# Optimization experiments

Hardware: AMD Instinct MI355X
Metric: run time of the kernel (lower is better)

The kernel has to match this reference:

```python
import jax, jax.numpy as jnp
import numpy as np

B, S, D, H, DK, DFF, L = 4, 1024, 1024, 16, 64, 4096, 128

def setup_inputs() -> dict:
    key = jax.random.key(0)
    ks = jax.random.split(key, 20)
    stdv = 1.0 / np.sqrt(D)
    u = lambda k, shape, s=stdv: jax.random.uniform(k, shape, jnp.float32, -s, s)
    x = jax.random.normal(ks[0], (B, S, D), jnp.float32)
    causal = jnp.triu(jnp.ones((S, S), bool), 1)          # True = masked
    attn_mask = jnp.broadcast_to(causal, (B, S, S))
    return {
        "x": x,
        "attn_mask": attn_mask,
        "W_q": u(ks[1], (H * DK, D)), "b_q": jnp.zeros((H * DK,)),
        "W_k": u(ks[2], (H * DK, D)), "b_k": jnp.zeros((H * DK,)),
        "W_v": u(ks[3], (H * DK, D)), "b_v": jnp.zeros((H * DK,)),
        "W_o": u(ks[4], (D, H * DK)), "b_o": jnp.zeros((D,)),
        "W_rel": u(ks[5], (2 * L + 1, DK), 1.0 / np.sqrt(DK)),
        "ln1_alpha": jnp.ones((D,)), "ln1_bias": jnp.zeros((D,)),
        "ln2_alpha": jnp.ones((D,)), "ln2_bias": jnp.zeros((D,)),
        "W1": u(ks[6], (DFF, D)), "b1": jnp.zeros((DFF,)),
        "W2": u(ks[7], (D, DFF)), "b2": jnp.zeros((D,)),
    }

def _layer_norm(x, alpha, bias, eps=1e-5):
    # Faithful to source: (x - mean) / (std + eps), std is biased (unbiased=False)
    m = jnp.mean(x, axis=-1, keepdims=True)
    std = jnp.sqrt(jnp.mean((x - m) ** 2, axis=-1, keepdims=True))
    return alpha * (x - m) / (std + eps) + bias

def reference(x, attn_mask, W_q, b_q, W_k, b_k, W_v, b_v, W_o, b_o, W_rel,
              ln1_alpha, ln1_bias, ln2_alpha, ln2_bias, W1, b1, W2, b2):
    b, s, d = x.shape
    q = (x @ W_q.T + b_q).reshape(b, s, H, DK)
    k = (x @ W_k.T + b_k).reshape(b, s, H, DK)
    v = (x @ W_v.T + b_v).reshape(b, s, H, DK)
    # relative position bias table lookup -> [s, s, DK]
    idx = jnp.clip(jnp.arange(s)[:, None] - jnp.arange(s)[None, :], -L, L) + L
    pos = W_rel[idx]
    # NOTE: original uses rel_pos_k_emb for BOTH pos_key and pos_value (as in source).
    scores = jnp.einsum('bqnd,bknd->bnqk', q, k) + jnp.einsum('bqnd,qkd->bnqk', q, pos)
    scores = scores / np.sqrt(DK)
    scores = jnp.where(attn_mask[:, None, :, :], jnp.float32(-10000.0), scores)
    attn = jax.nn.softmax(scores, axis=-1)
    out = jnp.einsum('bnqk,bknd->bnqd', attn, v) + jnp.einsum('bnqk,qkd->bnqd', attn, pos)
    out = out.transpose(0, 2, 1, 3).reshape(b, s, H * DK)
    out = out @ W_o.T + b_o
    # post-LN transformer layer: LN(x + attn), then LN(h + FFN(h))
    h = _layer_norm(x + out, ln1_alpha, ln1_bias)
    f = jax.nn.relu(h @ W1.T + b1) @ W2.T + b2
    return _layer_norm(h + f, ln2_alpha, ln2_bias)
```

## Files before the change

### kernel.cpp

```cpp
#include <hip/hip_runtime.h>
#include <cmath>
#include <cstdint>

typedef __bf16 bf16;
typedef __bf16 bf16x8 __attribute__((ext_vector_type(8)));
typedef __bf16 bf16x4 __attribute__((ext_vector_type(4)));
typedef float f32x4 __attribute__((ext_vector_type(4)));

__device__ __forceinline__ void async_ld16(const void* g, void* l) {
  __builtin_amdgcn_global_load_lds(
      (__attribute__((address_space(1))) void*)(uintptr_t)g,
      (__attribute__((address_space(3))) void*)l, 16, 0, 0);
}

__global__ void cast_kernel(const float* __restrict__ in, bf16* __restrict__ out, int n4) {
  int i = blockIdx.x * blockDim.x + threadIdx.x;
  if (i >= n4) return;
  float4 v = ((const float4*)in)[i];
  bf16x4 o; o[0]=(bf16)v.x; o[1]=(bf16)v.y; o[2]=(bf16)v.z; o[3]=(bf16)v.w;
  ((bf16x4*)out)[i] = o;
}

template<int BM>
__device__ __forceinline__ void gemm_core(
    const bf16* __restrict__ A, const bf16* __restrict__ Bm, const float* __restrict__ bias,
    float* __restrict__ outF, bf16* __restrict__ outB,
    const float* __restrict__ residF, const bf16* __restrict__ residB,
    int N, int K, int relu, bf16* As, bf16* Bs)
{
  constexpr int MI = BM / 32;
  const int tid  = threadIdx.x;
  const int wave = tid >> 6, lane = tid & 63;
  const int lr = lane & 15, lq = lane >> 4;
  const int bm = blockIdx.x * BM, bn = blockIdx.y * 128;
  const int wm = (wave >> 1) * (BM / 2), wn = (wave & 1) * 64;
  const int srow = lane >> 2, scol = (lane & 3) * 8;

  const f32x4 fz = {0.f, 0.f, 0.f, 0.f};
  f32x4 acc[MI][4];
#pragma unroll
  for (int i = 0; i < MI; i++)
#pragma unroll
    for (int j = 0; j < 4; j++) acc[i][j] = fz;

  for (int k0 = 0; k0 < K; k0 += 32) {
    __syncthreads();
    if (BM == 128) {
#pragma unroll
      for (int cc = 0; cc < 2; ++cc) {
        int c = wave * 2 + cc;
        async_ld16(A + (size_t)(bm + c * 16 + srow) * K + k0 + scol, As + c * 512);
      }
    } else {
      async_ld16(A + (size_t)(bm + wave * 16 + srow) * K + k0 + scol, As + wave * 512);
    }
#pragma unroll
    for (int cc = 0; cc < 2; ++cc) {
      int c = wave * 2 + cc;
      async_ld16(Bm + (size_t)(bn + c * 16 + srow) * K + k0 + scol, Bs + c * 512);
    }
    __syncthreads();
    bf16x8 af[MI], bfr[4];
#pragma unroll
    for (int mi = 0; mi < MI; mi++) af[mi]  = *(const bf16x8*)(As + (wm + mi*16 + lr)*32 + lq*8);
#pragma unroll
    for (int ni = 0; ni < 4; ni++) bfr[ni] = *(const bf16x8*)(Bs + (wn + ni*16 + lr)*32 + lq*8);
#pragma unroll
    for (int mi = 0; mi < MI; mi++)
#pragma unroll
      for (int ni = 0; ni < 4; ni++)
        acc[mi][ni] = __builtin_amdgcn_mfma_f32_16x16x32_bf16(af[mi], bfr[ni], acc[mi][ni], 0, 0, 0);
  }

#pragma unroll
  for (int ni = 0; ni < 4; ni++) {
    int n = bn + wn + ni*16 + lr;
    float bv = bias ? bias[n] : 0.0f;
#pragma unroll
    for (int mi = 0; mi < MI; mi++) {
#pragma unroll
      for (int r = 0; r < 4; r++) {
        int m = bm + wm + mi*16 + lq*4 + r;
        size_t idx = (size_t)m * N + n;
        float v = acc[mi][ni][r] + bv;
        if (relu) v = fmaxf(v, 0.0f);
        if (residF) v += residF[idx];
        if (residB) v += (float)residB[idx];
        if (outF) outF[idx] = v;
        else      outB[idx] = (bf16)v;
      }
    }
  }
}

template<int BM>
__global__ __launch_bounds__(256) void gemm_bt(
    const bf16* A, const bf16* Bm, const float* bias,
    float* outF, bf16* outB, const float* residF, const bf16* residB,
    int N, int K, int relu)
{
  __shared__ bf16 As[BM * 32];
  __shared__ bf16 Bs[128 * 32];
  gemm_core<BM>(A, Bm, bias, outF, outB, residF, residB, N, K, relu, As, Bs);
}

__global__ __launch_bounds__(256) void gemm_qkv(
    const bf16* A, const bf16* Bq, const bf16* Bk, const bf16* Bv,
    const float* bq, const float* bk, const float* bv,
    bf16* Oq, bf16* Ok, bf16* Ov, int N, int K)
{
  __shared__ bf16 As[128 * 32];
  __shared__ bf16 Bs[128 * 32];
  const bf16* Bm  = blockIdx.z == 0 ? Bq : (blockIdx.z == 1 ? Bk : Bv);
  const float* bi = blockIdx.z == 0 ? bq : (blockIdx.z == 1 ? bk : bv);
  bf16* O         = blockIdx.z == 0 ? Oq : (blockIdx.z == 1 ? Ok : Ov);
  gemm_core<128>(A, Bm, bi, nullptr, O, nullptr, nullptr, N, K, 0, As, Bs);
}

#define S_LEN 1024
#define ROWSTR 1024

__global__ __launch_bounds__(256) void attn_kernel(
    const bf16* __restrict__ Qg, const bf16* __restrict__ Kg, const bf16* __restrict__ Vg,
    const float* __restrict__ Wrel, bf16* __restrict__ Og)
{
  __shared__ __align__(16) bf16 hist[64][136];
  __shared__ __align__(16) bf16 rel_s[64][132];
  __shared__ __align__(16) bf16 ovl[13824];
  bf16* K_s = ovl;
  bf16* V_T = ovl + 4608;
  bf16* p_s = ovl + 9216;
  bf16* Wr_n = ovl;
  bf16* Wr_t = ovl;

  const int tid = threadIdx.x;
  const int wave = tid >> 6, lane = tid & 63;
  const int lr = lane & 15, lq = lane >> 4;
  const int qblk = 15 - blockIdx.x;
  const int b = blockIdx.y >> 4, h = blockIdx.y & 15;
  const int q0 = qblk * 64;
  const int T = qblk + 1;
  const int nearStart = (T > 3) ? T - 3 : 0;
  const size_t rowbase = (size_t)b * S_LEN * ROWSTR + h * 64;

  for (int e = tid; e < 144 * 64; e += 256) {
    int t = e >> 6, d = e & 63;
    float v = (t <= 128) ? Wrel[(size_t)(128 + t) * 64 + d] : 0.0f;
    Wr_n[t * 72 + d] = (bf16)v;
  }
  for (int e = tid; e < 64 * 68; e += 256) ((uint*)hist)[e] = 0u;

  const int qfrow = q0 + wave * 16 + lr;
  bf16x8 qf[2];
#pragma unroll
  for (int c = 0; c < 2; c++)
    qf[c] = *(const bf16x8*)(Qg + rowbase + (size_t)qfrow * ROWSTR + c * 32 + lq * 8);

  __syncthreads();

  const f32x4 fz = {0.f, 0.f, 0.f, 0.f};
#pragma unroll
  for (int tt = 0; tt < 9; ++tt) {
    f32x4 a = fz;
#pragma unroll
    for (int c = 0; c < 2; c++) {
      bf16x8 wf = *(const bf16x8*)(Wr_n + (tt * 16 + lr) * 72 + c * 32 + lq * 8);
      a = __builtin_amdgcn_mfma_f32_16x16x32_bf16(qf[c], wf, a, 0, 0, 0);
    }
    int t = tt * 16 + lr;
    if (t < 132) {
#pragma unroll
      for (int r = 0; r < 4; r++) rel_s[wave * 16 + lq * 4 + r][t] = (bf16)a[r];
    }
  }
  asm volatile("s_waitcnt lgkmcnt(0)" ::: "memory");
  float relc[4];
#pragma unroll
  for (int r = 0; r < 4; r++) relc[r] = 0.125f * (float)rel_s[wave * 16 + lq * 4 + r][128];

  float l_i[4], h128[4];
  f32x4 acc_o[4];
#pragma unroll
  for (int r = 0; r < 4; r++) { l_i[r] = 0.0f; h128[r] = 0.0f; }
#pragma unroll
  for (int dt = 0; dt < 4; dt++) acc_o[dt] = fz;
  const int qrow0 = q0 + wave * 16 + lq * 4;

  const int kr0 = tid >> 3, kc0 = (tid & 7) * 8;
  const int vr0 = 2 * (tid & 31), vd0 = (tid >> 5) * 8;
  uint4 ka, kb, va, vb;
  {
    const bf16* kp = Kg + rowbase + (size_t)kr0 * ROWSTR + kc0;
    ka = *(const uint4*)kp; kb = *(const uint4*)(kp + 32 * ROWSTR);
    const bf16* vp = Vg + rowbase + (size_t)vr0 * ROWSTR + vd0;
    va = *(const uint4*)vp; vb = *(const uint4*)(vp + ROWSTR);
  }

  for (int kt = 0; kt < T; ++kt) {
    const int k0 = kt * 64;
    __syncthreads();
    *(uint4*)(K_s + kr0 * 72 + kc0) = ka;
    *(uint4*)(K_s + (kr0 + 32) * 72 + kc0) = kb;
    {
      const ushort* pa = (const ushort*)&va;
      const ushort* pb = (const ushort*)&vb;
#pragma unroll
      for (int j = 0; j < 8; j++) {
        uint w = (uint)pa[j] | ((uint)pb[j] << 16);
        *(uint*)(V_T + (vd0 + j) * 72 + vr0) = w;
      }
    }
    __syncthreads();
    if (kt + 1 < T) {
      const bf16* kp = Kg + rowbase + (size_t)(k0 + 64 + kr0) * ROWSTR + kc0;
      ka = *(const uint4*)kp; kb = *(const uint4*)(kp + 32 * ROWSTR);
      const bf16* vp = Vg + rowbase + (size_t)(k0 + 64 + vr0) * ROWSTR + vd0;
      va = *(const uint4*)vp; vb = *(const uint4*)(vp + ROWSTR);
    }

    f32x4 sc[4];
#pragma unroll
    for (int nt = 0; nt < 4; nt++) {
      sc[nt] = fz;
#pragma unroll
      for (int c = 0; c < 2; c++) {
        bf16x8 kf = *(const bf16x8*)(K_s + (nt * 16 + lr) * 72 + c * 32 + lq * 8);
        sc[nt] = __builtin_amdgcn_mfma_f32_16x16x32_bf16(qf[c], kf, sc[nt], 0, 0, 0);
      }
    }

    float pw[4][4];
    if (kt < nearStart) {
#pragma unroll
      for (int nt = 0; nt < 4; nt++)
#pragma unroll
        for (int r = 0; r < 4; r++)
          pw[nt][r] = __expf(fmaf(sc[nt][r], 0.125f, relc[r]));
#pragma unroll
      for (int r = 0; r < 4; r++) {
        float s4 = pw[0][r] + pw[1][r] + pw[2][r] + pw[3][r];
        l_i[r] += s4; h128[r] += s4;
      }
    } else {
#pragma unroll
      for (int nt = 0; nt < 4; nt++) {
        int kg = k0 + nt * 16 + lr;
#pragma unroll
        for (int r = 0; r < 4; r++) {
          int qg = qrow0 + r;
          float p = 0.0f;
          if (kg <= qg) {
            int t = qg - kg; int tc = t > 128 ? 128 : t;
            p = __expf((sc[nt][r] + (float)rel_s[wave * 16 + lq * 4 + r][tc]) * 0.125f);
            l_i[r] += p;
            if (t >= 128) h128[r] += p;
            else          hist[wave * 16 + lq * 4 + r][t] = (bf16)p;
          }
          pw[nt][r] = p;
        }
      }
    }

#pragma unroll
    for (int nt = 0; nt < 4; nt++)
#pragma unroll
      for (int r = 0; r < 4; r++)
        p_s[(wave * 16 + lq * 4 + r) * 72 + nt * 16 + lr] = (bf16)pw[nt][r];
    asm volatile("s_waitcnt lgkmcnt(0)" ::: "memory");
#pragma unroll
    for (int c = 0; c < 2; c++) {
      bf16x8 pf = *(const bf16x8*)(p_s + (wave * 16 + lr) * 72 + c * 32 + lq * 8);
#pragma unroll
      for (int dt = 0; dt < 4; dt++) {
        bf16x8 vf = *(const bf16x8*)(V_T + (dt * 16 + lr) * 72 + c * 32 + lq * 8);
        acc_o[dt] = __builtin_amdgcn_mfma_f32_16x16x32_bf16(pf, vf, acc_o[dt], 0, 0, 0);
      }
    }
  }

  __syncthreads();
  for (int e = tid; e < 64 * 128; e += 256) {
    int d = e >> 7, t = e & 127;
    Wr_t[d * 136 + t] = (bf16)Wrel[(size_t)(128 + t) * 64 + d];
  }
  __syncthreads();
#pragma unroll
  for (int c = 0; c < 4; c++) {
    bf16x8 hf = *(const bf16x8*)&hist[wave * 16 + lr][c * 32 + lq * 8];
#pragma unroll
    for (int dt = 0; dt < 4; dt++) {
      bf16x8 wf = *(const bf16x8*)(Wr_t + (dt * 16 + lr) * 136 + c * 32 + lq * 8);
      acc_o[dt] = __builtin_amdgcn_mfma_f32_16x16x32_bf16(hf, wf, acc_o[dt], 0, 0, 0);
    }
  }
#pragma unroll
  for (int mk = 1; mk <= 8; mk <<= 1)
#pragma unroll
    for (int r = 0; r < 4; r++) {
      h128[r] += __shfl_xor(h128[r], mk);
      l_i[r]  += __shfl_xor(l_i[r],  mk);
    }
#pragma unroll
  for (int dt = 0; dt < 4; dt++) {
    float wv = Wrel[(size_t)256 * 64 + dt * 16 + lr];
#pragma unroll
    for (int r = 0; r < 4; r++) acc_o[dt][r] += h128[r] * wv;
  }
#pragma unroll
  for (int dt = 0; dt < 4; dt++)
#pragma unroll
    for (int r = 0; r < 4; r++) {
      int qg = qrow0 + r;
      float v = acc_o[dt][r] / l_i[r];
      Og[rowbase + (size_t)qg * ROWSTR + dt * 16 + lr] = (bf16)v;
    }
}

__global__ __launch_bounds__(256) void ln_kernel(
    const float* __restrict__ in, const float* __restrict__ alpha, const float* __restrict__ beta,
    float* __restrict__ outF, bf16* __restrict__ outB)
{
  const int row = blockIdx.x, tid = threadIdx.x;
  const int lane = tid & 63, wave = tid >> 6;
  float4 v = ((const float4*)(in + (size_t)row * 1024))[tid];
  float s  = v.x + v.y + v.z + v.w;
  float ss = v.x*v.x + v.y*v.y + v.z*v.z + v.w*v.w;
#pragma unroll
  for (int off = 32; off; off >>= 1) { s += __shfl_down(s, off); ss += __shfl_down(ss, off); }
  __shared__ float rs[4], rss[4];
  if (lane == 0) { rs[wave] = s; rss[wave] = ss; }
  __syncthreads();
  s  = rs[0] + rs[1] + rs[2] + rs[3];
  ss = rss[0] + rss[1] + rss[2] + rss[3];
  float mean = s * (1.0f / 1024.0f);
  float var  = ss * (1.0f / 1024.0f) - mean * mean;
  float inv  = 1.0f / (sqrtf(fmaxf(var, 0.0f)) + 1e-5f);
  float4 a = ((const float4*)alpha)[tid];
  float4 bb = ((const float4*)beta)[tid];
  float o0 = a.x * (v.x - mean) * inv + bb.x;
  float o1 = a.y * (v.y - mean) * inv + bb.y;
  float o2 = a.z * (v.z - mean) * inv + bb.z;
  float o3 = a.w * (v.w - mean) * inv + bb.w;
  if (outF) { float4 o = {o0, o1, o2, o3}; ((float4*)(outF + (size_t)row * 1024))[tid] = o; }
  if (outB) { bf16x4 o; o[0]=(bf16)o0; o[1]=(bf16)o1; o[2]=(bf16)o2; o[3]=(bf16)o3;
              ((bf16x4*)(outB + (size_t)row * 1024))[tid] = o; }
}

extern "C" void kernel_launch(void* const* d_in, const int* in_sizes, int n_in,
                              void* d_out, int out_size, void* d_ws, size_t ws_size,
                              hipStream_t stream) {
  (void)in_sizes; (void)n_in; (void)out_size; (void)ws_size;
  const int Mtok = 4096, D = 1024, DFF = 4096;

  const float* x    = (const float*)d_in[0];
  const float* Wq   = (const float*)d_in[2];
  const float* bq   = (const float*)d_in[3];
  const float* Wk   = (const float*)d_in[4];
  const float* bk   = (const float*)d_in[5];
  const float* Wv   = (const float*)d_in[6];
  const float* bv   = (const float*)d_in[7];
  const float* Wo   = (const float*)d_in[8];
  const float* bo   = (const float*)d_in[9];
  const float* Wrel = (const float*)d_in[10];
  const float* g1   = (const float*)d_in[11];
  const float* be1  = (const float*)d_in[12];
  const float* g2   = (const float*)d_in[13];
  const float* be2  = (const float*)d_in[14];
  const float* W1   = (const float*)d_in[15];
  const float* b1   = (const float*)d_in[16];
  const float* W2   = (const float*)d_in[17];
  const float* b2   = (const float*)d_in[18];

  char* ws = (char*)d_ws;
  const size_t MB = 1024 * 1024;
  bf16*  xb   = (bf16*)(ws + 0);
  bf16*  Wqb  = (bf16*)(ws + 8  * MB);
  bf16*  Wkb  = (bf16*)(ws + 10 * MB);
  bf16*  Wvb  = (bf16*)(ws + 12 * MB);
  bf16*  Wob  = (bf16*)(ws + 14 * MB);
  bf16*  W1b  = (bf16*)(ws + 16 * MB);
  bf16*  W2b  = (bf16*)(ws + 24 * MB);
  bf16*  Qb   = (bf16*)(ws + 32 * MB);
  bf16*  Kb   = (bf16*)(ws + 40 * MB);
  bf16*  Vb   = (bf16*)(ws + 48 * MB);
  bf16*  AOb  = (bf16*)(ws + 56 * MB);
  float* res1 = (float*)(ws + 64 * MB);
  bf16*  f1   = Qb;
  bf16*  hb   = xb;
  float* res2 = res1;

  cast_kernel<<<(Mtok * D / 4) / 256, 256, 0, stream>>>(x,  xb,  Mtok * D / 4);
  cast_kernel<<<(D * D / 4) / 256,    256, 0, stream>>>(Wq, Wqb, D * D / 4);
  cast_kernel<<<(D * D / 4) / 256,    256, 0, stream>>>(Wk, Wkb, D * D / 4);
  cast_kernel<<<(D * D / 4) / 256,    256, 0, stream>>>(Wv, Wvb, D * D / 4);
  cast_kernel<<<(D * D / 4) / 256,    256, 0, stream>>>(Wo, Wob, D * D / 4);
  cast_kernel<<<(DFF * D / 4) / 256,  256, 0, stream>>>(W1, W1b, DFF * D / 4);
  cast_kernel<<<(D * DFF / 4) / 256,  256, 0, stream>>>(W2, W2b, D * DFF / 4);

  gemm_qkv<<<dim3(32, 8, 3), 256, 0, stream>>>(xb, Wqb, Wkb, Wvb, bq, bk, bv, Qb, Kb, Vb, D, D);
  attn_kernel<<<dim3(16, 64), 256, 0, stream>>>(Qb, Kb, Vb, Wrel, AOb);
  gemm_bt<64><<<dim3(64, 8), 256, 0, stream>>>(AOb, Wob, bo, res1, nullptr, x, nullptr, D, D, 0);
  ln_kernel<<<Mtok, 256, 0, stream>>>(res1, g1, be1, nullptr, hb);
  gemm_bt<128><<<dim3(32, 32), 256, 0, stream>>>(hb, W1b, b1, nullptr, f1, nullptr, nullptr, DFF, D, 1);
  gemm_bt<64><<<dim3(64, 8), 256, 0, stream>>>(f1, W2b, b2, res2, nullptr, nullptr, hb, D, DFF, 0);
  ln_kernel<<<Mtok, 256, 0, stream>>>(res2, g2, be2, (float*)d_out, nullptr);
}
```

Before: 452.2 us.

## Split-K the N=1024 GEMMs into 128-row tiles and fuse reduction into LayerNorm

The output-projection and FFN-down GEMMs (N=1024) now run as a two-way split-K with 128-row tiles, writing two fp32 partial buffers. The LayerNorm kernel sums the partials and adds bias and residual before normalising, which replaces the old GEMM epilogue. All seven fp32-to-bf16 casts are merged into one launch. The intent is better MFMA tile efficiency and fewer launches, at the cost of an extra fp32 partial write and read per GEMM.

Result: faster. 417.5 us (-7.7%).

```diff
diff --git a/kernel.cpp b/kernel.cpp
--- a/kernel.cpp
+++ b/kernel.cpp
@@ -13,12 +13,25 @@
       (__attribute__((address_space(3))) void*)l, 16, 0, 0);
 }
 
-__global__ void cast_kernel(const float* __restrict__ in, bf16* __restrict__ out, int n4) {
-  int i = blockIdx.x * blockDim.x + threadIdx.x;
-  if (i >= n4) return;
-  float4 v = ((const float4*)in)[i];
+__global__ __launch_bounds__(256) void cast_all(
+    const float* __restrict__ x,  const float* __restrict__ wq, const float* __restrict__ wk,
+    const float* __restrict__ wv, const float* __restrict__ wo, const float* __restrict__ w1,
+    const float* __restrict__ w2,
+    bf16* xb, bf16* wqb, bf16* wkb, bf16* wvb, bf16* wob, bf16* w1b, bf16* w2b)
+{
+  int i = blockIdx.x * 256 + threadIdx.x;
+  const int M1 = 1 << 20, Q = 1 << 18;
+  const float* src; bf16* dst; int off;
+  if      (i < M1)            { src = x;  dst = xb;  off = i; }
+  else if (i < M1 + Q)        { src = wq; dst = wqb; off = i - M1; }
+  else if (i < M1 + 2 * Q)    { src = wk; dst = wkb; off = i - M1 - Q; }
+  else if (i < M1 + 3 * Q)    { src = wv; dst = wvb; off = i - M1 - 2 * Q; }
+  else if (i < M1 + 4 * Q)    { src = wo; dst = wob; off = i - M1 - 3 * Q; }
+  else if (i < 3 * M1)        { src = w1; dst = w1b; off = i - M1 - 4 * Q; }
+  else                        { src = w2; dst = w2b; off = i - 3 * M1; }
+  float4 v = ((const float4*)src)[off];
   bf16x4 o; o[0]=(bf16)v.x; o[1]=(bf16)v.y; o[2]=(bf16)v.z; o[3]=(bf16)v.w;
-  ((bf16x4*)out)[i] = o;
+  ((bf16x4*)dst)[off] = o;
 }
 
 template<int BM>
@@ -26,7 +39,7 @@
     const bf16* __restrict__ A, const bf16* __restrict__ Bm, const float* __restrict__ bias,
     float* __restrict__ outF, bf16* __restrict__ outB,
     const float* __restrict__ residF, const bf16* __restrict__ residB,
-    int N, int K, int relu, bf16* As, bf16* Bs)
+    int N, int kld, int kbeg, int kend, int relu, bf16* As, bf16* Bs)
 {
   constexpr int MI = BM / 32;
   const int tid  = threadIdx.x;
@@ -43,21 +56,21 @@
 #pragma unroll
     for (int j = 0; j < 4; j++) acc[i][j] = fz;
 
-  for (int k0 = 0; k0 < K; k0 += 32) {
+  for (int k0 = kbeg; k0 < kend; k0 += 32) {
     __syncthreads();
     if (BM == 128) {
 #pragma unroll
       for (int cc = 0; cc < 2; ++cc) {
         int c = wave * 2 + cc;
-        async_ld16(A + (size_t)(bm + c * 16 + srow) * K + k0 + scol, As + c * 512);
+        async_ld16(A + (size_t)(bm + c * 16 + srow) * kld + k0 + scol, As + c * 512);
       }
     } else {
-      async_ld16(A + (size_t)(bm + wave * 16 + srow) * K + k0 + scol, As + wave * 512);
+      async_ld16(A + (size_t)(bm + wave * 16 + srow) * kld + k0 + scol, As + wave * 512);
     }
 #pragma unroll
     for (int cc = 0; cc < 2; ++cc) {
       int c = wave * 2 + cc;
-      async_ld16(Bm + (size_t)(bn + c * 16 + srow) * K + k0 + scol, Bs + c * 512);
+      async_ld16(Bm + (size_t)(bn + c * 16 + srow) * kld + k0 + scol, Bs + c * 512);
     }
     __syncthreads();
     bf16x8 af[MI], bfr[4];
@@ -101,7 +114,17 @@
 {
   __shared__ bf16 As[BM * 32];
   __shared__ bf16 Bs[128 * 32];
-  gemm_core<BM>(A, Bm, bias, outF, outB, residF, residB, N, K, relu, As, Bs);
+  gemm_core<BM>(A, Bm, bias, outF, outB, residF, residB, N, K, 0, K, relu, As, Bs);
+}
+
+__global__ __launch_bounds__(256) void gemm_splitk(
+    const bf16* A, const bf16* Bm, float* part, int N, int kld, int kchunk)
+{
+  __shared__ bf16 As[128 * 32];
+  __shared__ bf16 Bs[128 * 32];
+  const int z = blockIdx.z;
+  gemm_core<128>(A, Bm, nullptr, part + (size_t)z * 4096 * N, nullptr, nullptr, nullptr,
+                 N, kld, z * kchunk, (z + 1) * kchunk, 0, As, Bs);
 }
 
 __global__ __launch_bounds__(256) void gemm_qkv(
@@ -114,7 +137,7 @@
   const bf16* Bm  = blockIdx.z == 0 ? Bq : (blockIdx.z == 1 ? Bk : Bv);
   const float* bi = blockIdx.z == 0 ? bq : (blockIdx.z == 1 ? bk : bv);
   bf16* O         = blockIdx.z == 0 ? Oq : (blockIdx.z == 1 ? Ok : Ov);
-  gemm_core<128>(A, Bm, bi, nullptr, O, nullptr, nullptr, N, K, 0, As, Bs);
+  gemm_core<128>(A, Bm, bi, nullptr, O, nullptr, nullptr, N, K, 0, K, 0, As, Bs);
 }
 
 #define S_LEN 1024
@@ -316,13 +339,29 @@
     }
 }
 
-__global__ __launch_bounds__(256) void ln_kernel(
-    const float* __restrict__ in, const float* __restrict__ alpha, const float* __restrict__ beta,
+__global__ __launch_bounds__(256) void ln_fuse(
+    const float* __restrict__ pA, const float* __restrict__ pB,
+    const float* __restrict__ bias,
+    const float* __restrict__ residF, const bf16* __restrict__ residB,
+    const float* __restrict__ alpha, const float* __restrict__ beta,
     float* __restrict__ outF, bf16* __restrict__ outB)
 {
   const int row = blockIdx.x, tid = threadIdx.x;
   const int lane = tid & 63, wave = tid >> 6;
-  float4 v = ((const float4*)(in + (size_t)row * 1024))[tid];
+  const size_t base = (size_t)row * 1024;
+  float4 v = ((const float4*)(pA + base))[tid];
+  float4 v2 = ((const float4*)(pB + base))[tid];
+  v.x += v2.x; v.y += v2.y; v.z += v2.z; v.w += v2.w;
+  float4 bv = ((const float4*)bias)[tid];
+  v.x += bv.x; v.y += bv.y; v.z += bv.z; v.w += bv.w;
+  if (residF) {
+    float4 rv = ((const float4*)(residF + base))[tid];
+    v.x += rv.x; v.y += rv.y; v.z += rv.z; v.w += rv.w;
+  }
+  if (residB) {
+    bf16x4 rv = ((const bf16x4*)(residB + base))[tid];
+    v.x += (float)rv[0]; v.y += (float)rv[1]; v.z += (float)rv[2]; v.w += (float)rv[3];
+  }
   float s  = v.x + v.y + v.z + v.w;
   float ss = v.x*v.x + v.y*v.y + v.z*v.z + v.w*v.w;
 #pragma unroll
@@ -341,16 +380,16 @@
   float o1 = a.y * (v.y - mean) * inv + bb.y;
   float o2 = a.z * (v.z - mean) * inv + bb.z;
   float o3 = a.w * (v.w - mean) * inv + bb.w;
-  if (outF) { float4 o = {o0, o1, o2, o3}; ((float4*)(outF + (size_t)row * 1024))[tid] = o; }
+  if (outF) { float4 o = {o0, o1, o2, o3}; ((float4*)(outF + base))[tid] = o; }
   if (outB) { bf16x4 o; o[0]=(bf16)o0; o[1]=(bf16)o1; o[2]=(bf16)o2; o[3]=(bf16)o3;
-              ((bf16x4*)(outB + (size_t)row * 1024))[tid] = o; }
+              ((bf16x4*)(outB + base))[tid] = o; }
 }
 
 extern "C" void kernel_launch(void* const* d_in, const int* in_sizes, int n_in,
                               void* d_out, int out_size, void* d_ws, size_t ws_size,
                               hipStream_t stream) {
   (void)in_sizes; (void)n_in; (void)out_size; (void)ws_size;
-  const int Mtok = 4096, D = 1024, DFF = 4096;
+  const int D = 1024, DFF = 4096;
 
   const float* x    = (const float*)d_in[0];
   const float* Wq   = (const float*)d_in[2];
@@ -384,24 +423,18 @@
   bf16*  Kb   = (bf16*)(ws + 40 * MB);
   bf16*  Vb   = (bf16*)(ws + 48 * MB);
   bf16*  AOb  = (bf16*)(ws + 56 * MB);
-  float* res1 = (float*)(ws + 64 * MB);
+  float* part = (float*)(ws + 64 * MB);
   bf16*  f1   = Qb;
   bf16*  hb   = xb;
-  float* res2 = res1;
-
-  cast_kernel<<<(Mtok * D / 4) / 256, 256, 0, stream>>>(x,  xb,  Mtok * D / 4);
-  cast_kernel<<<(D * D / 4) / 256,    256, 0, stream>>>(Wq, Wqb, D * D / 4);
-  cast_kernel<<<(D * D / 4) / 256,    256, 0, stream>>>(Wk, Wkb, D * D / 4);
-  cast_kernel<<<(D * D / 4) / 256,    256, 0, stream>>>(Wv, Wvb, D * D / 4);
-  cast_kernel<<<(D * D / 4) / 256,    256, 0, stream>>>(Wo, Wob, D * D / 4);
-  cast_kernel<<<(DFF * D / 4) / 256,  256, 0, stream>>>(W1, W1b, DFF * D / 4);
-  cast_kernel<<<(D * DFF / 4) / 256,  256, 0, stream>>>(W2, W2b, D * DFF / 4);
+
+  cast_all<<<16384, 256, 0, stream>>>(x, Wq, Wk, Wv, Wo, W1, W2,
+                                      xb, Wqb, Wkb, Wvb, Wob, W1b, W2b);
 
   gemm_qkv<<<dim3(32, 8, 3), 256, 0, stream>>>(xb, Wqb, Wkb, Wvb, bq, bk, bv, Qb, Kb, Vb, D, D);
   attn_kernel<<<dim3(16, 64), 256, 0, stream>>>(Qb, Kb, Vb, Wrel, AOb);
-  gemm_bt<64><<<dim3(64, 8), 256, 0, stream>>>(AOb, Wob, bo, res1, nullptr, x, nullptr, D, D, 0);
-  ln_kernel<<<Mtok, 256, 0, stream>>>(res1, g1, be1, nullptr, hb);
+  gemm_splitk<<<dim3(32, 8, 2), 256, 0, stream>>>(AOb, Wob, part, D, D, 512);
+  ln_fuse<<<4096, 256, 0, stream>>>(part, part + 4096 * 1024, bo, x, nullptr, g1, be1, nullptr, hb);
   gemm_bt<128><<<dim3(32, 32), 256, 0, stream>>>(hb, W1b, b1, nullptr, f1, nullptr, nullptr, DFF, D, 1);
-  gemm_bt<64><<<dim3(64, 8), 256, 0, stream>>>(f1, W2b, b2, res2, nullptr, nullptr, hb, D, DFF, 0);
-  ln_kernel<<<Mtok, 256, 0, stream>>>(res2, g2, be2, (float*)d_out, nullptr);
-}
+  gemm_splitk<<<dim3(32, 8, 2), 256, 0, stream>>>(f1, W2b, part, D, DFF, 2048);
+  ln_fuse<<<4096, 256, 0, stream>>>(part, part + 4096 * 1024, b2, nullptr, hb, g2, be2, (float*)d_out, nullptr);
+}
```
